# Kernel optimization log

Hardware: AMD Instinct MI355X
Metric: run time of the kernel (lower is better)

## Reference

```python
import jax, jax.numpy as jnp
import numpy as np

H = 2048    # hidden_size
NH = 16     # num q heads
NKV = 8     # num kv heads
HD = 128    # head_dim
S = 2048    # seq len
FF = 8192   # intermediate_size
EPS = 1e-6


def setup_inputs() -> dict:
    key = jax.random.key(0)
    ks = jax.random.split(key, 14)
    sc = 0.02
    w = lambda k, shape: jax.random.normal(k, shape, jnp.float32) * sc
    # rotary tables (standard rotate-half RoPE)
    inv_freq = 1.0 / (10000.0 ** (jnp.arange(0, HD, 2, dtype=jnp.float32) / HD))
    freqs = jnp.outer(jnp.arange(S, dtype=jnp.float32), inv_freq)
    emb = jnp.concatenate([freqs, freqs], axis=-1)  # [S, HD]
    return {
        'hidden_states': jax.random.normal(ks[0], (1, S, H), jnp.float32),
        'cos': jnp.cos(emb),
        'sin': jnp.sin(emb),
        'wq': w(ks[1], (H, NH * HD)),
        'wk': w(ks[2], (H, NKV * HD)),
        'wv': w(ks[3], (H, NKV * HD)),
        'wo': w(ks[4], (NH * HD, H)),
        'w1': w(ks[5], (H, FF)),
        'w3': w(ks[6], (H, FF)),
        'w2': w(ks[7], (FF, H)),
        'v1': w(ks[8], (H, FF)),
        'v3': w(ks[9], (H, FF)),
        'v2': w(ks[10], (FF, H)),
        'attn_norm_w': jnp.ones((H,), jnp.float32),
        'ffn_norm_w': jnp.ones((H,), jnp.float32),
        'vision_idx': jnp.arange(1024, dtype=jnp.int32),          # first half = vision tokens
        'text_idx': jnp.arange(1024, dtype=jnp.int32) + 1024,     # second half = text tokens
    }


def _rmsnorm(x, w):
    var = jnp.mean(jnp.square(x), axis=-1, keepdims=True)
    return x * jax.lax.rsqrt(var + EPS) * w


def _rotate_half(x):
    x1, x2 = jnp.split(x, 2, axis=-1)
    return jnp.concatenate([-x2, x1], axis=-1)


def _mlp(x, wg, wu, wd):
    # InternLM2MLP: w2(silu(w1(x)) * w3(x))
    return (jax.nn.silu(x @ wg) * (x @ wu)) @ wd


def reference(hidden_states, cos, sin, wq, wk, wv, wo, w1, w3, w2,
              v1, v3, v2, attn_norm_w, ffn_norm_w, vision_idx, text_idx):
    B = hidden_states.shape[0]
    # residual is None -> residual = hidden_states; h = attention_norm(h)
    residual = hidden_states
    h = _rmsnorm(hidden_states, attn_norm_w)

    # --- attention (GQA + RoPE, causal, no kv cache) ---
    q = (h @ wq).reshape(B, S, NH, HD)
    k = (h @ wk).reshape(B, S, NKV, HD)
    v = (h @ wv).reshape(B, S, NKV, HD)
    c = cos[None, :, None, :]
    s = sin[None, :, None, :]
    q = q * c + _rotate_half(q) * s
    k = k * c + _rotate_half(k) * s
    rep = NH // NKV
    k = jnp.repeat(k, rep, axis=2)  # [B,S,NH,HD]
    v = jnp.repeat(v, rep, axis=2)
    scores = jnp.einsum('bqhd,bkhd->bhqk', q, k) / np.sqrt(HD).astype(np.float32)
    causal = jnp.tril(jnp.ones((S, S), dtype=bool))
    scores = jnp.where(causal[None, None], scores, jnp.finfo(scores.dtype).min)
    probs = jax.nn.softmax(scores, axis=-1)
    attn = jnp.einsum('bhqk,bkhd->bqhd', probs, v).reshape(B, S, NH * HD)
    attn = attn @ wo

    # --- fused ffn_norm(hidden, residual): residual += hidden; h = norm(residual) ---
    residual = residual + attn
    h = _rmsnorm(residual, ffn_norm_w)

    # --- dual-expert dispatch: vision tokens -> feed_forward_ve, text -> feed_forward ---
    h_vis = _mlp(h[:, vision_idx, :], v1, v3, v2)
    h_txt = _mlp(h[:, text_idx, :], w1, w3, w2)
    out = h.at[:, vision_idx, :].set(h_vis).at[:, text_idx, :].set(h_txt)
    return out, residual
```

## Files before the change

kernel.cpp:

```cpp
#include <hip/hip_runtime.h>


typedef __bf16 bf16_t;
typedef __bf16 bf16x8 __attribute__((ext_vector_type(8)));
typedef float f32x4 __attribute__((ext_vector_type(4)));

#define GLOAD16(gp, lp)                                                     \
  __builtin_amdgcn_global_load_lds(                                         \
      (__attribute__((address_space(1))) void*)(unsigned long long)(gp),    \
      (__attribute__((address_space(3))) void*)(lp), 16, 0, 0)

__global__ __launch_bounds__(256) void transpose_k(const float* __restrict__ W,
                                                   bf16_t* __restrict__ Wt,
                                                   int K, int N, int row_off) {
  __shared__ bf16_t tile[32][34];
  const int tx = threadIdx.x & 31, ty = threadIdx.x >> 5;
  const int n0 = blockIdx.x * 32, k0 = blockIdx.y * 32;
#pragma unroll
  for (int i = 0; i < 4; i++)
    tile[ty + 8 * i][tx] = (bf16_t)W[(size_t)(k0 + ty + 8 * i) * N + n0 + tx];
  __syncthreads();
#pragma unroll
  for (int i = 0; i < 4; i++)
    Wt[(size_t)(row_off + n0 + ty + 8 * i) * K + k0 + tx] = tile[tx][ty + 8 * i];
}

__global__ __launch_bounds__(256) void transpose_bf16_k(
    const bf16_t* __restrict__ in, int ldin, bf16_t* __restrict__ out, int ldout) {
  __shared__ bf16_t tile[32][34];
  const int tx = threadIdx.x & 31, ty = threadIdx.x >> 5;
  const int c0 = blockIdx.x * 32, r0 = blockIdx.y * 32;
#pragma unroll
  for (int i = 0; i < 4; i++)
    tile[ty + 8 * i][tx] = in[(size_t)(r0 + ty + 8 * i) * ldin + c0 + tx];
  __syncthreads();
#pragma unroll
  for (int i = 0; i < 4; i++)
    out[(size_t)(c0 + ty + 8 * i) * ldout + r0 + tx] = tile[tx][ty + 8 * i];
}

__global__ __launch_bounds__(256) void rmsnorm_k(const float* __restrict__ x,
                                                 const float* __restrict__ w,
                                                 bf16_t* __restrict__ y) {
  const int row = blockIdx.x, t = threadIdx.x;
  __shared__ float red[256];
  float vals[8];
  float ss = 0.f;
  const float* xr = x + (size_t)row * 2048;
#pragma unroll
  for (int i = 0; i < 8; i++) {
    float v = xr[t + 256 * i];
    vals[i] = v;
    ss += v * v;
  }
  red[t] = ss;
  __syncthreads();
  for (int s = 128; s > 0; s >>= 1) {
    if (t < s) red[t] += red[t + s];
    __syncthreads();
  }
  const float scale = rsqrtf(red[0] * (1.f / 2048.f) + 1e-6f);
  bf16_t* yr = y + (size_t)row * 2048;
#pragma unroll
  for (int i = 0; i < 8; i++)
    yr[t + 256 * i] = (bf16_t)(vals[i] * scale * w[t + 256 * i]);
}

__global__ __launch_bounds__(128) void rope_k(bf16_t* __restrict__ qkv,
                                              const float* __restrict__ cosb,
                                              const float* __restrict__ sinb) {
  const int s = blockIdx.x, head = blockIdx.y, d = threadIdx.x;
  bf16_t* p = qkv + (size_t)s * 4096 + head * 128;
  const float x = (float)p[d];
  const float partner = (float)p[d ^ 64];
  const float rot = (d < 64) ? -partner : partner;
  const float c = cosb[s * 128 + d], sn = sinb[s * 128 + d];
  __syncthreads();
  p[d] = (bf16_t)(x * c + rot * sn);
}

__global__ __launch_bounds__(256) void attn_mfma_k(
    const bf16_t* __restrict__ qkv,
    const bf16_t* __restrict__ vt,
    bf16_t* __restrict__ ob) {
  __shared__ __align__(16) bf16_t Ks[64][136];
  __shared__ __align__(16) bf16_t Vs[128][72];
  __shared__ __align__(16) bf16_t Ps[4][16][72];

  const int t = threadIdx.x;
  const int wid = t >> 6, lane = t & 63;
  const int lr = lane & 15, lg = lane >> 4;
  const int h = blockIdx.y, kvh = h >> 1;
  const int qt = (int)gridDim.x - 1 - (int)blockIdx.x;
  const int q0 = qt * 64;
  const int nkb = qt + 1;
  const int qrow_base = q0 + wid * 16;

  bf16x8 qf[4];
#pragma unroll
  for (int cs = 0; cs < 4; ++cs)
    qf[cs] = *(const bf16x8*)(qkv + (size_t)(qrow_base + lr) * 4096 + h * 128 +
                              lg * 8 + 32 * cs);

  f32x4 acc[8];
#pragma unroll
  for (int dt = 0; dt < 8; ++dt) acc[dt] = f32x4{0.f, 0.f, 0.f, 0.f};
  float m_run[4] = {-1e30f, -1e30f, -1e30f, -1e30f};
  float l_run[4] = {0.f, 0.f, 0.f, 0.f};

  const float SCALE = 0.08838834764831845f;

  for (int kb = 0; kb < nkb; ++kb) {
    const int k0 = kb * 64;
    __syncthreads();
#pragma unroll
    for (int i = 0; i < 4; ++i) {
      const int v = t + 256 * i;
      const int kr = v >> 4, c = (v & 15) * 8;
      *(bf16x8*)&Ks[kr][c] =
          *(const bf16x8*)(qkv + (size_t)(k0 + kr) * 4096 + 2048 + kvh * 128 + c);
    }
#pragma unroll
    for (int i = 0; i < 4; ++i) {
      const int v = t + 256 * i;
      const int d = v >> 3, kk = (v & 7) * 8;
      *(bf16x8*)&Vs[d][kk] =
          *(const bf16x8*)(vt + (size_t)(kvh * 128 + d) * 2048 + k0 + kk);
    }
    __syncthreads();

    f32x4 sv[4];
#pragma unroll
    for (int t4 = 0; t4 < 4; ++t4) sv[t4] = f32x4{0.f, 0.f, 0.f, 0.f};
#pragma unroll
    for (int cs = 0; cs < 4; ++cs) {
#pragma unroll
      for (int t4 = 0; t4 < 4; ++t4) {
        const bf16x8 kf = *(const bf16x8*)&Ks[16 * t4 + lr][lg * 8 + 32 * cs];
        sv[t4] = __builtin_amdgcn_mfma_f32_16x16x32_bf16(qf[cs], kf, sv[t4], 0, 0, 0);
      }
    }

    const bool need_mask = (k0 + 63) > qrow_base;
#pragma unroll
    for (int t4 = 0; t4 < 4; ++t4) {
#pragma unroll
      for (int r = 0; r < 4; ++r) {
        float x = sv[t4][r] * SCALE;
        if (need_mask && (k0 + 16 * t4 + lr) > (qrow_base + 4 * lg + r)) x = -1e30f;
        sv[t4][r] = x;
      }
    }

#pragma unroll
    for (int r = 0; r < 4; ++r) {
      float mx = fmaxf(fmaxf(sv[0][r], sv[1][r]), fmaxf(sv[2][r], sv[3][r]));
      mx = fmaxf(mx, __shfl_xor(mx, 1));
      mx = fmaxf(mx, __shfl_xor(mx, 2));
      mx = fmaxf(mx, __shfl_xor(mx, 4));
      mx = fmaxf(mx, __shfl_xor(mx, 8));
      const float mnew = fmaxf(m_run[r], mx);
      const float corr = __expf(m_run[r] - mnew);
      m_run[r] = mnew;
      float ls = 0.f;
#pragma unroll
      for (int t4 = 0; t4 < 4; ++t4) {
        const float p = __expf(sv[t4][r] - mnew);
        ls += p;
        Ps[wid][4 * lg + r][16 * t4 + lr] = (bf16_t)p;
      }
      ls += __shfl_xor(ls, 1);
      ls += __shfl_xor(ls, 2);
      ls += __shfl_xor(ls, 4);
      ls += __shfl_xor(ls, 8);
      l_run[r] = l_run[r] * corr + ls;
#pragma unroll
      for (int dt = 0; dt < 8; ++dt) acc[dt][r] *= corr;
    }

#pragma unroll
    for (int ks = 0; ks < 2; ++ks) {
      const bf16x8 pa = *(const bf16x8*)&Ps[wid][lr][lg * 8 + 32 * ks];
#pragma unroll
      for (int dt = 0; dt < 8; ++dt) {
        const bf16x8 vf = *(const bf16x8*)&Vs[16 * dt + lr][lg * 8 + 32 * ks];
        acc[dt] = __builtin_amdgcn_mfma_f32_16x16x32_bf16(pa, vf, acc[dt], 0, 0, 0);
      }
    }
  }

#pragma unroll
  for (int r = 0; r < 4; ++r) {
    const float inv = 1.f / l_run[r];
    const size_t row = (size_t)(qrow_base + 4 * lg + r) * 2048 + h * 128;
#pragma unroll
    for (int dt = 0; dt < 8; ++dt)
      ob[row + 16 * dt + lr] = (bf16_t)(acc[dt][r] * inv);
  }
}

__global__ __launch_bounds__(256) void gemm_bt(
    const bf16_t* __restrict__ A, int lda, const int* __restrict__ a_idx,
    const bf16_t* __restrict__ Bt, int K,
    float* __restrict__ Cf, bf16_t* __restrict__ Cb,
    const int* __restrict__ c_idx, int ldc, int mode,
    const bf16_t* __restrict__ Gb, const float* __restrict__ Rf) {
  __shared__ __align__(16) bf16_t As[128 * 32];
  __shared__ __align__(16) bf16_t Bs[128 * 32];
  __shared__ int arows[128];

  const int t = threadIdx.x;
  const int row0 = blockIdx.y * 128, col0 = blockIdx.x * 128;

  if (t < 128) arows[t] = a_idx ? a_idx[row0 + t] : (row0 + t);
  __syncthreads();

  const int sm0 = t >> 2;
  const int sq0 = (((t & 3) ^ ((sm0 >> 1) & 3)) << 3);
  const int sm1 = (t + 256) >> 2;
  const int sq1 = ((((t + 256) & 3) ^ ((sm1 >> 1) & 3)) << 3);

  const bf16_t* gA0 = A + (size_t)arows[sm0] * lda + sq0;
  const bf16_t* gA1 = A + (size_t)arows[sm1] * lda + sq1;
  const bf16_t* gB0 = Bt + (size_t)(col0 + sm0) * K + sq0;
  const bf16_t* gB1 = Bt + (size_t)(col0 + sm1) * K + sq1;

  const int wid = t >> 6, lane = t & 63;
  bf16_t* ldsA0 = As + wid * 512;
  bf16_t* ldsA1 = As + 2048 + wid * 512;
  bf16_t* ldsB0 = Bs + wid * 512;
  bf16_t* ldsB1 = Bs + 2048 + wid * 512;

  const int wm = (wid & 1) << 6, wn = (wid >> 1) << 6;
  const int lrow = lane & 15, lq = lane >> 4;

  int a_off[4], b_off[4];
#pragma unroll
  for (int i = 0; i < 4; i++) {
    const int m = wm + i * 16 + lrow;
    a_off[i] = m * 64 + ((lq ^ ((m >> 1) & 3)) << 4);
    const int n = wn + i * 16 + lrow;
    b_off[i] = n * 64 + ((lq ^ ((n >> 1) & 3)) << 4);
  }

  f32x4 acc[4][4];
#pragma unroll
  for (int i = 0; i < 4; i++)
#pragma unroll
    for (int j = 0; j < 4; j++) acc[i][j] = f32x4{0.f, 0.f, 0.f, 0.f};

  for (int k0 = 0; k0 < K; k0 += 32) {
    __syncthreads();
    GLOAD16(gA0 + k0, ldsA0);
    GLOAD16(gA1 + k0, ldsA1);
    GLOAD16(gB0 + k0, ldsB0);
    GLOAD16(gB1 + k0, ldsB1);
    __syncthreads();
    bf16x8 af[4], bfr[4];
#pragma unroll
    for (int i = 0; i < 4; i++)
      af[i] = *(const bf16x8*)((const char*)As + a_off[i]);
#pragma unroll
    for (int i = 0; i < 4; i++)
      bfr[i] = *(const bf16x8*)((const char*)Bs + b_off[i]);
#pragma unroll
    for (int i = 0; i < 4; i++)
#pragma unroll
      for (int j = 0; j < 4; j++)
        acc[i][j] =
            __builtin_amdgcn_mfma_f32_16x16x32_bf16(af[i], bfr[j], acc[i][j], 0, 0, 0);
  }

#pragma unroll
  for (int i = 0; i < 4; i++) {
#pragma unroll
    for (int r = 0; r < 4; r++) {
      const int gm = row0 + wm + i * 16 + lq * 4 + r;
      const int crow = c_idx ? c_idx[gm] : gm;
      const size_t base = (size_t)crow * ldc;
#pragma unroll
      for (int j = 0; j < 4; j++) {
        const int col = col0 + wn + j * 16 + lrow;
        float v = acc[i][j][r];
        if (mode == 0) {
          Cf[base + col] = v;
        } else if (mode == 1) {
          Cf[base + col] = v + Rf[base + col];
        } else if (mode == 2) {
          const float g = (float)Gb[base + col];
          Cb[base + col] = (bf16_t)(v * g / (1.f + __expf(-g)));
        } else {
          Cb[base + col] = (bf16_t)v;
        }
      }
    }
  }
}

extern "C" void kernel_launch(void* const* d_in, const int* in_sizes, int n_in,
                              void* d_out, int out_size, void* d_ws, size_t ws_size,
                              hipStream_t stream) {
  const float* hidden = (const float*)d_in[0];
  const float* cosb = (const float*)d_in[1];
  const float* sinb = (const float*)d_in[2];
  const float* wq = (const float*)d_in[3];
  const float* wk = (const float*)d_in[4];
  const float* wv = (const float*)d_in[5];
  const float* wo = (const float*)d_in[6];
  const float* w1 = (const float*)d_in[7];
  const float* w3 = (const float*)d_in[8];
  const float* w2 = (const float*)d_in[9];
  const float* v1 = (const float*)d_in[10];
  const float* v3 = (const float*)d_in[11];
  const float* v2 = (const float*)d_in[12];
  const float* anw = (const float*)d_in[13];
  const float* fnw = (const float*)d_in[14];
  const int* vidx = (const int*)d_in[15];
  const int* tidx = (const int*)d_in[16];

  float* out0 = (float*)d_out;
  float* outr = out0 + (size_t)2048 * 2048;

  char* wsb = (char*)d_ws;
  const size_t MB = 1024 * 1024;
  bf16_t* qkvb = (bf16_t*)(wsb + 0 * MB);
  bf16_t* vt = (bf16_t*)(wsb + 16 * MB);
  bf16_t* attnb = (bf16_t*)(wsb + 24 * MB);
  bf16_t* hn = (bf16_t*)(wsb + 32 * MB);
  bf16_t* g = (bf16_t*)(wsb + 0 * MB);
  bf16_t* act = (bf16_t*)(wsb + 16 * MB);
  bf16_t* bufT = (bf16_t*)(wsb + 40 * MB);

  transpose_k<<<dim3(64, 64), 256, 0, stream>>>(wq, bufT, 2048, 2048, 0);
  transpose_k<<<dim3(32, 64), 256, 0, stream>>>(wk, bufT, 2048, 1024, 2048);
  transpose_k<<<dim3(32, 64), 256, 0, stream>>>(wv, bufT, 2048, 1024, 3072);
  rmsnorm_k<<<2048, 256, 0, stream>>>(hidden, anw, hn);
  gemm_bt<<<dim3(32, 16), 256, 0, stream>>>(hn, 2048, nullptr, bufT, 2048, nullptr,
                                            qkvb, nullptr, 4096, 3, nullptr, nullptr);
  rope_k<<<dim3(2048, 24), 128, 0, stream>>>(qkvb, cosb, sinb);
  transpose_bf16_k<<<dim3(32, 64), 256, 0, stream>>>(qkvb + 3072, 4096, vt, 2048);
  attn_mfma_k<<<dim3(32, 16), 256, 0, stream>>>(qkvb, vt, attnb);
  transpose_k<<<dim3(64, 64), 256, 0, stream>>>(wo, bufT, 2048, 2048, 0);
  gemm_bt<<<dim3(16, 16), 256, 0, stream>>>(attnb, 2048, nullptr, bufT, 2048, outr,
                                            nullptr, nullptr, 2048, 1, nullptr, hidden);
  rmsnorm_k<<<2048, 256, 0, stream>>>(outr, fnw, hn);
  const float* Wg[2] = {v1, w1};
  const float* Wu[2] = {v3, w3};
  const float* Wd[2] = {v2, w2};
  const int* idx[2] = {vidx, tidx};
  for (int hh = 0; hh < 2; hh++) {
    transpose_k<<<dim3(256, 64), 256, 0, stream>>>(Wg[hh], bufT, 2048, 8192, 0);
    gemm_bt<<<dim3(64, 8), 256, 0, stream>>>(hn, 2048, idx[hh], bufT, 2048, nullptr,
                                             g, nullptr, 8192, 3, nullptr, nullptr);
    transpose_k<<<dim3(256, 64), 256, 0, stream>>>(Wu[hh], bufT, 2048, 8192, 0);
    gemm_bt<<<dim3(64, 8), 256, 0, stream>>>(hn, 2048, idx[hh], bufT, 2048, nullptr,
                                             act, nullptr, 8192, 2, g, nullptr);
    transpose_k<<<dim3(64, 256), 256, 0, stream>>>(Wd[hh], bufT, 8192, 2048, 0);
    gemm_bt<<<dim3(16, 8), 256, 0, stream>>>(act, 8192, nullptr, bufT, 8192, out0,
                                             nullptr, idx[hh], 2048, 0, nullptr,
                                             nullptr);
  }
}
```

Baseline: 1.366 ms.

## Halve GEMM N-tile and add split-K with atomic accumulation for small grids

The GEMM tile shrinks from 128x128 to 128x64, doubling block counts. Split-K across gridDim.z is added, with fp32 atomicAdd into a pre-initialised output: a residual copy for the wo projection and a zeroed buffer for the down projections. The intent is to fill more compute units on the small-grid GEMMs, which previously launched only 128-256 blocks. In exchange it adds copy and zero kernels, atomic traffic, a non-deterministic summation order, halved reuse of A per block, and it reorders the FFN stages and reuses the output buffer as scratch for the gate activations.

```diff
diff --git a/kernel.cpp b/kernel.cpp
--- a/kernel.cpp
+++ b/kernel.cpp
@@ -37,6 +37,17 @@
 #pragma unroll
   for (int i = 0; i < 4; i++)
     out[(size_t)(c0 + ty + 8 * i) * ldout + r0 + tx] = tile[tx][ty + 8 * i];
+}
+
+__global__ __launch_bounds__(256) void fcopy_k(const float4* __restrict__ s,
+                                               float4* __restrict__ d, int n) {
+  for (int i = blockIdx.x * 256 + threadIdx.x; i < n; i += gridDim.x * 256)
+    d[i] = s[i];
+}
+__global__ __launch_bounds__(256) void fzero_k(float4* __restrict__ d, int n) {
+  const float4 z = {0.f, 0.f, 0.f, 0.f};
+  for (int i = blockIdx.x * 256 + threadIdx.x; i < n; i += gridDim.x * 256)
+    d[i] = z;
 }
 
 __global__ __launch_bounds__(256) void rmsnorm_k(const float* __restrict__ x,
@@ -204,13 +215,15 @@
     const bf16_t* __restrict__ Bt, int K,
     float* __restrict__ Cf, bf16_t* __restrict__ Cb,
     const int* __restrict__ c_idx, int ldc, int mode,
-    const bf16_t* __restrict__ Gb, const float* __restrict__ Rf) {
+    const bf16_t* __restrict__ Gb) {
   __shared__ __align__(16) bf16_t As[128 * 32];
-  __shared__ __align__(16) bf16_t Bs[128 * 32];
+  __shared__ __align__(16) bf16_t Bs[64 * 32];
   __shared__ int arows[128];
 
   const int t = threadIdx.x;
-  const int row0 = blockIdx.y * 128, col0 = blockIdx.x * 128;
+  const int row0 = blockIdx.y * 128, col0 = blockIdx.x * 64;
+  const int kpz = K / (int)gridDim.z;
+  const int kbeg = blockIdx.z * kpz, kend = kbeg + kpz;
 
   if (t < 128) arows[t] = a_idx ? a_idx[row0 + t] : (row0 + t);
   __syncthreads();
@@ -219,54 +232,56 @@
   const int sq0 = (((t & 3) ^ ((sm0 >> 1) & 3)) << 3);
   const int sm1 = (t + 256) >> 2;
   const int sq1 = ((((t + 256) & 3) ^ ((sm1 >> 1) & 3)) << 3);
+  const int bn0 = t >> 2;
+  const int bq0 = (((t & 3) ^ ((bn0 >> 1) & 3)) << 3);
 
   const bf16_t* gA0 = A + (size_t)arows[sm0] * lda + sq0;
   const bf16_t* gA1 = A + (size_t)arows[sm1] * lda + sq1;
-  const bf16_t* gB0 = Bt + (size_t)(col0 + sm0) * K + sq0;
-  const bf16_t* gB1 = Bt + (size_t)(col0 + sm1) * K + sq1;
+  const bf16_t* gB0 = Bt + (size_t)(col0 + bn0) * K + bq0;
 
   const int wid = t >> 6, lane = t & 63;
   bf16_t* ldsA0 = As + wid * 512;
   bf16_t* ldsA1 = As + 2048 + wid * 512;
   bf16_t* ldsB0 = Bs + wid * 512;
-  bf16_t* ldsB1 = Bs + 2048 + wid * 512;
-
-  const int wm = (wid & 1) << 6, wn = (wid >> 1) << 6;
+
+  const int wm = (wid & 1) << 6, wn = (wid >> 1) << 5;
   const int lrow = lane & 15, lq = lane >> 4;
 
-  int a_off[4], b_off[4];
+  int a_off[4], b_off[2];
 #pragma unroll
   for (int i = 0; i < 4; i++) {
     const int m = wm + i * 16 + lrow;
     a_off[i] = m * 64 + ((lq ^ ((m >> 1) & 3)) << 4);
-    const int n = wn + i * 16 + lrow;
-    b_off[i] = n * 64 + ((lq ^ ((n >> 1) & 3)) << 4);
-  }
-
-  f32x4 acc[4][4];
-#pragma unroll
-  for (int i = 0; i < 4; i++)
-#pragma unroll
-    for (int j = 0; j < 4; j++) acc[i][j] = f32x4{0.f, 0.f, 0.f, 0.f};
-
-  for (int k0 = 0; k0 < K; k0 += 32) {
+  }
+#pragma unroll
+  for (int j = 0; j < 2; j++) {
+    const int n = wn + j * 16 + lrow;
+    b_off[j] = n * 64 + ((lq ^ ((n >> 1) & 3)) << 4);
+  }
+
+  f32x4 acc[4][2];
+#pragma unroll
+  for (int i = 0; i < 4; i++)
+#pragma unroll
+    for (int j = 0; j < 2; j++) acc[i][j] = f32x4{0.f, 0.f, 0.f, 0.f};
+
+  for (int k0 = kbeg; k0 < kend; k0 += 32) {
     __syncthreads();
     GLOAD16(gA0 + k0, ldsA0);
     GLOAD16(gA1 + k0, ldsA1);
     GLOAD16(gB0 + k0, ldsB0);
-    GLOAD16(gB1 + k0, ldsB1);
-    __syncthreads();
-    bf16x8 af[4], bfr[4];
+    __syncthreads();
+    bf16x8 af[4], bfr[2];
 #pragma unroll
     for (int i = 0; i < 4; i++)
       af[i] = *(const bf16x8*)((const char*)As + a_off[i]);
 #pragma unroll
+    for (int j = 0; j < 2; j++)
+      bfr[j] = *(const bf16x8*)((const char*)Bs + b_off[j]);
+#pragma unroll
     for (int i = 0; i < 4; i++)
-      bfr[i] = *(const bf16x8*)((const char*)Bs + b_off[i]);
-#pragma unroll
-    for (int i = 0; i < 4; i++)
-#pragma unroll
-      for (int j = 0; j < 4; j++)
+#pragma unroll
+      for (int j = 0; j < 2; j++)
         acc[i][j] =
             __builtin_amdgcn_mfma_f32_16x16x32_bf16(af[i], bfr[j], acc[i][j], 0, 0, 0);
   }
@@ -279,13 +294,11 @@
       const int crow = c_idx ? c_idx[gm] : gm;
       const size_t base = (size_t)crow * ldc;
 #pragma unroll
-      for (int j = 0; j < 4; j++) {
+      for (int j = 0; j < 2; j++) {
         const int col = col0 + wn + j * 16 + lrow;
         float v = acc[i][j][r];
         if (mode == 0) {
-          Cf[base + col] = v;
-        } else if (mode == 1) {
-          Cf[base + col] = v + Rf[base + col];
+          atomicAdd(Cf + base + col, v);
         } else if (mode == 2) {
           const float g = (float)Gb[base + col];
           Cb[base + col] = (bf16_t)(v * g / (1.f + __expf(-g)));
@@ -327,22 +340,26 @@
   bf16_t* vt = (bf16_t*)(wsb + 16 * MB);
   bf16_t* attnb = (bf16_t*)(wsb + 24 * MB);
   bf16_t* hn = (bf16_t*)(wsb + 32 * MB);
-  bf16_t* g = (bf16_t*)(wsb + 0 * MB);
-  bf16_t* act = (bf16_t*)(wsb + 16 * MB);
+  bf16_t* act = (bf16_t*)(wsb + 0 * MB);
   bf16_t* bufT = (bf16_t*)(wsb + 40 * MB);
-
+  bf16_t* gbuf = (bf16_t*)out0;
+
+  fcopy_k<<<2048, 256, 0, stream>>>((const float4*)hidden, (float4*)outr,
+                                    2048 * 2048 / 4);
   transpose_k<<<dim3(64, 64), 256, 0, stream>>>(wq, bufT, 2048, 2048, 0);
   transpose_k<<<dim3(32, 64), 256, 0, stream>>>(wk, bufT, 2048, 1024, 2048);
   transpose_k<<<dim3(32, 64), 256, 0, stream>>>(wv, bufT, 2048, 1024, 3072);
   rmsnorm_k<<<2048, 256, 0, stream>>>(hidden, anw, hn);
-  gemm_bt<<<dim3(32, 16), 256, 0, stream>>>(hn, 2048, nullptr, bufT, 2048, nullptr,
-                                            qkvb, nullptr, 4096, 3, nullptr, nullptr);
+  gemm_bt<<<dim3(64, 16, 1), 256, 0, stream>>>(hn, 2048, nullptr, bufT, 2048,
+                                               nullptr, qkvb, nullptr, 4096, 3,
+                                               nullptr);
   rope_k<<<dim3(2048, 24), 128, 0, stream>>>(qkvb, cosb, sinb);
   transpose_bf16_k<<<dim3(32, 64), 256, 0, stream>>>(qkvb + 3072, 4096, vt, 2048);
   attn_mfma_k<<<dim3(32, 16), 256, 0, stream>>>(qkvb, vt, attnb);
   transpose_k<<<dim3(64, 64), 256, 0, stream>>>(wo, bufT, 2048, 2048, 0);
-  gemm_bt<<<dim3(16, 16), 256, 0, stream>>>(attnb, 2048, nullptr, bufT, 2048, outr,
-                                            nullptr, nullptr, 2048, 1, nullptr, hidden);
+  gemm_bt<<<dim3(32, 16, 2), 256, 0, stream>>>(attnb, 2048, nullptr, bufT, 2048,
+                                               outr, nullptr, nullptr, 2048, 0,
+                                               nullptr);
   rmsnorm_k<<<2048, 256, 0, stream>>>(outr, fnw, hn);
   const float* Wg[2] = {v1, w1};
   const float* Wu[2] = {v3, w3};
@@ -350,14 +367,19 @@
   const int* idx[2] = {vidx, tidx};
   for (int hh = 0; hh < 2; hh++) {
     transpose_k<<<dim3(256, 64), 256, 0, stream>>>(Wg[hh], bufT, 2048, 8192, 0);
-    gemm_bt<<<dim3(64, 8), 256, 0, stream>>>(hn, 2048, idx[hh], bufT, 2048, nullptr,
-                                             g, nullptr, 8192, 3, nullptr, nullptr);
+    gemm_bt<<<dim3(128, 8, 1), 256, 0, stream>>>(hn, 2048, idx[hh], bufT, 2048,
+                                                 nullptr, gbuf, nullptr, 8192, 3,
+                                                 nullptr);
     transpose_k<<<dim3(256, 64), 256, 0, stream>>>(Wu[hh], bufT, 2048, 8192, 0);
-    gemm_bt<<<dim3(64, 8), 256, 0, stream>>>(hn, 2048, idx[hh], bufT, 2048, nullptr,
-                                             act, nullptr, 8192, 2, g, nullptr);
+    gemm_bt<<<dim3(128, 8, 1), 256, 0, stream>>>(
+        hn, 2048, idx[hh], bufT, 2048, nullptr, act + (size_t)hh * 1024 * 8192,
+        nullptr, 8192, 2, gbuf);
+  }
+  fzero_k<<<2048, 256, 0, stream>>>((float4*)out0, 2048 * 2048 / 4);
+  for (int hh = 0; hh < 2; hh++) {
     transpose_k<<<dim3(64, 256), 256, 0, stream>>>(Wd[hh], bufT, 8192, 2048, 0);
-    gemm_bt<<<dim3(16, 8), 256, 0, stream>>>(act, 8192, nullptr, bufT, 8192, out0,
-                                             nullptr, idx[hh], 2048, 0, nullptr,
-                                             nullptr);
-  }
-}
+    gemm_bt<<<dim3(32, 8, 4), 256, 0, stream>>>(
+        act + (size_t)hh * 1024 * 8192, 8192, nullptr, bufT, 8192, out0, nullptr,
+        idx[hh], 2048, 0, nullptr);
+  }
+}
```

Result: faster. 1.193 ms (-12.6%).
